# Kernel optimization log

Measured on AMD Instinct MI355X. Metric: run time of the kernel, lower is better.

Reference implementation:

```python
import jax, jax.numpy as jnp
from jax import lax
import numpy as np

# ----- static optical constants (from config) -----
N = 500            # phase mask grid
PX = 1e-6          # pixel pitch [m]
WL = 532e-9        # wavelength [m]
FL = 0.1           # focal length [m]
RI = 1.0           # refractive index
FWHC = 150e-6      # laser beam FWHC
K = 2.0 * np.pi * RI / WL
QE, DARK_MEAN, READ_STD, GAIN, MAX_ADU = 0.9, 0.005, 1.6, 2.0, 65535.0
MAX_VAL = 4.0e9    # Normalize01 max
PHOTONS = 1.0e6    # photons per emitter (max_intensity-style scaling)
R = 15             # psf_keep_radius -> 31x31 crops

_x = np.arange(-N // 2, N // 2) * PX
_X, _Y = np.meshgrid(_x, _x)
INCIDENT = np.exp(-(_X**2 + _Y**2) / (2.0 * FWHC**2)).astype(np.float32)
_C1 = (np.pi / (WL * FL) * (_X**2 + _Y**2)) % (2.0 * np.pi)
B1 = np.exp(-1j * _C1).astype(np.complex64)
# angular-spectrum gamma, directly in unshifted fft order
_F = np.fft.fftfreq(N, d=PX)
_A, _B = np.meshgrid(RI * WL * _F, RI * WL * _F)
GAMMA = np.sqrt(np.maximum(1.0 - _A**2 - _B**2, 0.0)).astype(np.float32)

def _gauss7():
    m = (7 - 1) / 2.0
    y, x = np.ogrid[-m:m + 1, -m:m + 1]
    h = np.exp(-(x * x + y * y) / 2.0)
    h[h < np.finfo(h.dtype).eps * h.max()] = 0
    return h.astype(np.float32)
GAUSS7 = _gauss7()


def setup_inputs() -> dict:
    key = jax.random.key(0)
    k1, k2, k3, k4, k5, k6, k7 = jax.random.split(key, 7)
    B, Ne = 8, 64
    phase_mask = jax.random.uniform(k1, (N, N), jnp.float32, 0.0, 2.0 * np.pi)
    zs = jax.random.uniform(k2, (Ne,), jnp.float32, 0.0, 1e-4)  # defocus depths [m]
    xyz = jax.random.randint(k3, (B, Ne, 2), 0, 170, jnp.int32) + 15  # in [15,184]
    std_u = jax.random.uniform(k4, (1,), jnp.float32)
    eps_dark = jax.random.normal(k5, (B, 1, 198, 198), jnp.float32)
    eps_photon = jax.random.normal(k6, (B, 1, 198, 198), jnp.float32)
    eps_read = jax.random.normal(k7, (B, 1, 198, 198), jnp.float32)
    return {"phase_mask": phase_mask, "zs": zs, "xyz": xyz, "std_u": std_u,
            "eps_dark": eps_dark, "eps_photon": eps_photon, "eps_read": eps_read}


def _forward(phase_mask, zs, xyz, std_u, eps_dark, eps_photon, eps_read):
    Bn, Ne = xyz.shape[0], xyz.shape[1]
    # --- FFT-based PSF generation (angular spectrum propagation) ---
    field = (INCIDENT * jnp.exp(1j * phase_mask) * B1).astype(jnp.complex64)  # [N,N]
    Ef = jnp.fft.fft2(field)                                                  # [N,N]
    H = jnp.exp(1j * ((K * GAMMA)[None] * zs[:, None, None]))                 # [Ne,N,N]
    Eprop = jnp.fft.ifft2(Ef[None] * H)                                       # [Ne,N,N]
    inten = jnp.abs(Eprop) ** 2
    c = N // 2
    psf = inten[:, c - R:c + R + 1, c - R:c + R + 1]                          # [Ne,31,31]
    psf = psf / (jnp.sum(psf, (-2, -1), keepdims=True) + 1e-12) * PHOTONS
    images4D = jnp.broadcast_to(psf[None], (Bn, Ne, 2 * R + 1, 2 * R + 1))
    # --- imgs4dto3d: scatter-add 31x31 patches into 200x200 canvas ---
    offs = jnp.arange(2 * R + 1) - R
    rows = xyz[..., 0][..., None, None] + offs[None, None, :, None]           # [B,Ne,31,1]
    cols = xyz[..., 1][..., None, None] + offs[None, None, None, :]           # [B,Ne,1,31]
    bidx = jnp.arange(Bn)[:, None, None, None]
    canvas = jnp.zeros((Bn, 200, 200), psf.dtype).at[bidx, rows, cols].add(images4D)
    img = canvas[:, None]                                                     # [B,1,200,200]
    # --- BlurLayer: per-draw std gaussian, conv pad=2 -> 198x198 ---
    std = 0.8 + 0.4 * std_u[0]
    s2 = std * std
    kern = (1.0 / (2.0 * jnp.pi * s2)) * GAUSS7 ** (1.0 / s2)
    blurred = lax.conv_general_dilated(img, kern[None, None], (1, 1),
                                       [(2, 2), (2, 2)],
                                       dimension_numbers=("NCHW", "OIHW", "NCHW"))
    # --- NoiseLayer (reparameterized gaussian approximations) ---
    sig = blurred * QE
    dark = DARK_MEAN + eps_dark * jnp.sqrt(jnp.float32(DARK_MEAN))
    total = jnp.maximum(sig + dark, 0.0)
    noisy = total + eps_photon * jnp.sqrt(jnp.maximum(total, 1e-12))
    elec = noisy + eps_read * READ_STD
    adu = jnp.clip(elec * GAIN, 0.0, MAX_ADU)
    # --- Normalize01 ---
    out = jnp.where(adu <= 10.0, 1.0, jnp.minimum(adu, MAX_VAL)) / MAX_VAL
    return out.astype(jnp.float32)


def reference(phase_mask, zs, xyz, std_u, eps_dark, eps_photon, eps_read):
    return _forward(phase_mask, zs, xyz, std_u, eps_dark, eps_photon, eps_read)
```

## Files before the change

kernel.cpp:

```cpp
#include <hip/hip_runtime.h>
#include <math.h>

#define NN 500
#define NE 64
#define BATCH 8
#define RR 15
#define PW 31
#define CAN 200
#define OHW 198
#define TWO_PI_F 6.28318530717958647692f
#define SETUP_N (BATCH * CAN * CAN + NE + 49)

#define BG2_F16 (64 * 2 * 2 * 64 * 8)
#define ASCALE (1.0f / 64.0f)

using f16x8 = __attribute__((ext_vector_type(8))) _Float16;
using f32x16 = __attribute__((ext_vector_type(16))) float;

__device__ __forceinline__ void fast_sincos_red(float theta, float* s, float* c) {
    const float INV2PI = 0.15915494309189535f;
    const float PI2_HI = 6.28318548202514648f;
    const float PI2_LO = -1.7484556e-7f;
    float n = rintf(theta * INV2PI);
    float r = fmaf(n, -PI2_HI, theta);
    r = fmaf(n, -PI2_LO, r);
    *s = __sinf(r);
    *c = __cosf(r);
}

__global__ void k_setup(const float* __restrict__ std_u,
                        float* __restrict__ kgamma,
                        float2* __restrict__ tw,
                        float* __restrict__ kern,
                        float* __restrict__ canvas,
                        float* __restrict__ psf_sums,
                        _Float16* __restrict__ Bg2) {
    int idx = blockIdx.x * blockDim.x + threadIdx.x;
    if (idx < NN) {
        double th = 2.0 * M_PI * (double)idx / (double)NN;
        tw[idx] = make_float2((float)cos(th), (float)sin(th));
    }
    if (idx < BG2_F16) {
        int e = idx & 7;
        int lane = (idx >> 3) & 63;
        int nt = (idx >> 9) & 1;
        int plane = (idx >> 10) & 1;
        int gs = idx >> 11;
        int kap = gs * 16 + (lane >> 5) * 8 + e;
        int nu = nt * 32 + (lane & 31);
        float outv = 0.f;
        if (kap < 2 * NN) {
            int u = kap >> 1, p = kap & 1;
            int ri = nu >> 1, q = nu & 1;
            int r = 235 + ri;
            int m = (u * r) % NN;
            double th = 2.0 * M_PI * (double)m / (double)NN;
            double wre = cos(th), wim = sin(th);
            double val = (q == 0) ? ((p == 0) ? wre : -wim)
                                  : ((p == 0) ? wim : wre);
            float x = (float)val;
            _Float16 h = (_Float16)x;
            outv = (plane == 0) ? (float)h : (x - (float)h);
        }
        Bg2[idx] = (_Float16)outv;
    }
    if (idx < BATCH * CAN * CAN) canvas[idx] = 0.f;
    if (idx >= BATCH * CAN * CAN && idx < BATCH * CAN * CAN + NE)
        psf_sums[idx - BATCH * CAN * CAN] = 0.f;
    if (idx >= BATCH * CAN * CAN + NE && idx < SETUP_N) {
        int t = idx - (BATCH * CAN * CAN + NE);
        float stdv = 0.8f + 0.4f * std_u[0];
        float s2 = stdv * stdv;
        int a = t / 7 - 3, b = t % 7 - 3;
        float g = (float)exp(-0.5 * (double)(a * a + b * b));
        kern[t] = (1.0f / (2.0f * (float)M_PI * s2)) * powf(g, 1.0f / s2);
    }
    if (idx >= NN * NN) return;
    int i = idx / NN, j = idx % NN;
    double fy = (double)((i < 250) ? i : i - 500) * 2000.0;
    double fx = (double)((j < 250) ? j : j - 500) * 2000.0;
    double a = 5.32e-7 * fx;
    double b = 5.32e-7 * fy;
    double g = 1.0 - a * a - b * b;
    g = (g > 0.0) ? sqrt(g) : 0.0;
    float Kf = (float)(2.0 * M_PI * 1.0 / 5.32e-7);
    kgamma[idx] = Kf * (float)g;
}

__device__ __forceinline__ void ct_dft_stages(const float2* xs, const float2* tts,
                                              float2* S, int t,
                                              float2* out1, float2* out2, int* kout) {
    if (t < 250) {
        int d = t / 25;
        int b = t % 25;
        float2 st = tts[(25 * d) % NN];
        float wr = 1.f, wi = 0.f;
        float Er = 0.f, Ei = 0.f, Or_ = 0.f, Oi = 0.f;
#pragma unroll
        for (int a = 0; a < 20; a += 2) {
            float2 x0 = xs[25 * a + b];
            Er += x0.x * wr - x0.y * wi;
            Ei += x0.x * wi + x0.y * wr;
            float nr = wr * st.x - wi * st.y;
            float ni = wr * st.y + wi * st.x;
            float2 x1 = xs[25 * (a + 1) + b];
            Or_ += x1.x * nr - x1.y * ni;
            Oi  += x1.x * ni + x1.y * nr;
            wr = nr * st.x - ni * st.y;
            wi = nr * st.y + ni * st.x;
        }
        S[b * 21 + d]      = make_float2(Er + Or_, Ei + Oi);
        S[b * 21 + d + 10] = make_float2(Er - Or_, Ei - Oi);
    }
    __syncthreads();
    if (t < 250) {
        int k = t;
        int d1 = k % 20;
        int d2 = (d1 + 10) % 20;
        float2 s1 = tts[k];
        float wr = 1.f, wi = 0.f;
        float a1r = 0.f, a1i = 0.f, a2r = 0.f, a2i = 0.f;
#pragma unroll
        for (int b = 0; b < 25; ++b) {
            float2 u1 = S[b * 21 + d1];
            float2 u2 = S[b * 21 + d2];
            a1r += u1.x * wr - u1.y * wi;
            a1i += u1.x * wi + u1.y * wr;
            float sgnb = (b & 1) ? -1.f : 1.f;
            float w2r = sgnb * wr, w2i = sgnb * wi;
            a2r += u2.x * w2r - u2.y * w2i;
            a2i += u2.x * w2i + u2.y * w2r;
            float nr = wr * s1.x - wi * s1.y;
            wi = wr * s1.y + wi * s1.x;
            wr = nr;
        }
        *out1 = make_float2(a1r, a1i);
        *out2 = make_float2(a2r, a2i);
        *kout = k;
    }
}

__global__ void k_dft_rows(const float* __restrict__ phase, float2* __restrict__ dst,
                           const float2* __restrict__ tw) {
    __shared__ __align__(16) float2 xs[NN];
    __shared__ float2 tts[NN];
    __shared__ float2 S[25 * 21];
    int line = blockIdx.x;
    int t = threadIdx.x;
    const float INV2SIG = 2.2222222e7f;
    const float C1M = (float)(M_PI / 5.32e-8);
    float y = (float)(line - 250) * 1e-6f;
    float y2 = y * y;
    const float* prow = phase + (size_t)line * NN;
    for (int n = t; n < NN; n += 256) {
        float x = (float)(n - 250) * 1e-6f;
        float r2 = x * x + y2;
        float inc = __expf(-r2 * INV2SIG);
        float c1 = C1M * r2;
        float b1r = __cosf(c1), b1i = -__sinf(c1);
        float ph = prow[n];
        float sp = __sinf(ph), cp = __cosf(ph);
        float ar = inc * cp, ai = inc * sp;
        xs[n] = make_float2(ar * b1r - ai * b1i, ar * b1i + ai * b1r);
        float2 tt = tw[n];
        tts[n] = make_float2(tt.x, -tt.y);
    }
    __syncthreads();
    float2 o1, o2; int k;
    ct_dft_stages(xs, tts, S, t, &o1, &o2, &k);
    if (t < 250) {
        dst[(size_t)k * NN + line] = o1;
        dst[(size_t)(k + 250) * NN + line] = o2;
    }
}

__global__ void k_dft_cols(const float2* __restrict__ src, float2* __restrict__ dst,
                           const float2* __restrict__ tw) {
    __shared__ __align__(16) float2 xs[NN];
    __shared__ float2 tts[NN];
    __shared__ float2 S[25 * 21];
    int line = blockIdx.x;
    const float2* s = src + (size_t)line * NN;
    int t = threadIdx.x;
    for (int n = t; n < NN; n += 256) {
        xs[n] = s[n];
        float2 tt = tw[n];
        tts[n] = make_float2(tt.x, -tt.y);
    }
    __syncthreads();
    float2 o1, o2; int k;
    ct_dft_stages(xs, tts, S, t, &o1, &o2, &k);
    if (t < 250) {
        float2* dp = dst + (size_t)line * NN;
        dp[k] = o1;
        dp[k + 250] = o2;
    }
}

__global__ void __launch_bounds__(256)
k_prop_mfma(const float2* __restrict__ EfT,
            const float* __restrict__ kgamma,
            const float* __restrict__ zs,
            const _Float16* __restrict__ Bg2,
            float* __restrict__ part) {
    __shared__ __align__(16) char smem[4 * 2048 * 4];
    float2* eft = (float2*)smem;
    float*  kgs = (float*)(smem + 4096);
    float*  ctile4 = (float*)smem;

    int v = blockIdx.x;
    int zh = blockIdx.y;
    int t = threadIdx.x;
    int w = t >> 6;
    int lane = t & 63;
    int l31 = lane & 31;
    int lk = lane >> 5;

    for (int n = t; n < 512; n += 256) {
        if (n < NN) {
            float2 e = EfT[(size_t)v * NN + n];
            eft[n] = make_float2(e.x * ASCALE, e.y * ASCALE);
            kgs[n] = kgamma[(size_t)v * NN + n];
        } else {
            eft[n] = make_float2(0.f, 0.f);
            kgs[n] = 0.f;
        }
    }
    float zv = zs[zh * 32 + l31];
    __syncthreads();

    f32x16 acc[2] = {};

#define MODSPLIT(ex, ey, kgv, i0) do {                                        \
        float s_, c_;                                                         \
        fast_sincos_red((kgv) * zv, &s_, &c_);                                \
        float yr = (ex) * c_ - (ey) * s_;                                     \
        float yi = (ex) * s_ + (ey) * c_;                                     \
        _Float16 h0 = (_Float16)yr;                                           \
        ah[i0] = h0; al[i0] = (_Float16)(yr - (float)h0);                     \
        _Float16 h1 = (_Float16)yi;                                           \
        ah[i0 + 1] = h1; al[i0 + 1] = (_Float16)(yi - (float)h1);             \
    } while (0)

    const _Float16* bbase = Bg2 + (size_t)(w * 16) * 2048 + (size_t)lane * 8;
#pragma unroll 4
    for (int s = 0; s < 16; ++s) {
        const _Float16* bs = bbase + (size_t)s * 2048;
        f16x8 bh0 = *(const f16x8*)(bs);
        f16x8 bh1 = *(const f16x8*)(bs + 512);
        f16x8 bl0 = *(const f16x8*)(bs + 1024);
        f16x8 bl1 = *(const f16x8*)(bs + 1536);
        int u0 = w * 128 + s * 8 + lk * 4;
        f16x8 ah, al;
        {
            float4 e01 = *(const float4*)&eft[u0];
            float4 e23 = *(const float4*)&eft[u0 + 2];
            float4 kg4 = *(const float4*)&kgs[u0];
            MODSPLIT(e01.x, e01.y, kg4.x, 0);
            MODSPLIT(e01.z, e01.w, kg4.y, 2);
            MODSPLIT(e23.x, e23.y, kg4.z, 4);
            MODSPLIT(e23.z, e23.w, kg4.w, 6);
        }
        acc[0] = __builtin_amdgcn_mfma_f32_32x32x16_f16(ah, bh0, acc[0], 0, 0, 0);
        acc[0] = __builtin_amdgcn_mfma_f32_32x32x16_f16(al, bh0, acc[0], 0, 0, 0);
        acc[0] = __builtin_amdgcn_mfma_f32_32x32x16_f16(ah, bl0, acc[0], 0, 0, 0);
        acc[1] = __builtin_amdgcn_mfma_f32_32x32x16_f16(ah, bh1, acc[1], 0, 0, 0);
        acc[1] = __builtin_amdgcn_mfma_f32_32x32x16_f16(al, bh1, acc[1], 0, 0, 0);
        acc[1] = __builtin_amdgcn_mfma_f32_32x32x16_f16(ah, bl1, acc[1], 0, 0, 0);
    }
#undef MODSPLIT

    __syncthreads();
    {
        float* slice = ctile4 + w * 2048;
#pragma unroll
        for (int nt = 0; nt < 2; ++nt)
#pragma unroll
            for (int reg = 0; reg < 16; ++reg) {
                int row = (reg & 3) + 8 * (reg >> 2) + 4 * lk;
                slice[row * 64 + nt * 32 + l31] = acc[nt][reg];
            }
    }
    __syncthreads();
#pragma unroll
    for (int pass = 0; pass < 2; ++pass) {
        int idx = pass * 256 + t;
        int i4 = idx * 4;
        int z = i4 >> 6, c4 = (i4 & 63) >> 2;
        float4 a0 = *(const float4*)&ctile4[i4];
        float4 a1 = *(const float4*)&ctile4[2048 + i4];
        float4 a2 = *(const float4*)&ctile4[4096 + i4];
        float4 a3 = *(const float4*)&ctile4[6144 + i4];
        float4 val = make_float4(a0.x + a1.x + a2.x + a3.x,
                                 a0.y + a1.y + a2.y + a3.y,
                                 a0.z + a1.z + a2.z + a3.z,
                                 a0.w + a1.w + a2.w + a3.w);
        *(float4*)&part[((size_t)(zh * 32 + z) * NN + v) * 64 + c4 * 4] = val;
    }
}

__global__ void k_prop_cols(const float* __restrict__ part,
                            float* __restrict__ psf,
                            float* __restrict__ psf_sums) {
    __shared__ __align__(16) float X2[NN][16];
    int rq = blockIdx.x;
    int z  = blockIdx.y;
    int t  = threadIdx.x;
    const float* p0 = part + ((size_t)z * NN) * 64 + rq * 16;
    for (int i = t; i < NN * 4; i += 256) {
        int v = i >> 2, q4 = i & 3;
        float4 a = *(const float4*)(p0 + (size_t)v * 64 + q4 * 4);
        *(float4*)&X2[v][q4 * 4] = a;
    }
    __syncthreads();
    int ril = t >> 5;
    int ri  = rq * 8 + ril;
    int ci  = t & 31;
    float val = 0.f;
    if (ri < PW && ci < PW) {
        int c = 235 + ci;
        float ar = 0.f, ai = 0.f;
        float sr, si;
        {
            float th = (TWO_PI_F / NN) * (float)(c % NN);
            sincosf(th, &si, &sr);
        }
        for (int vb = 0; vb < 4; ++vb) {
            int v0 = vb * 125;
            float wr, wi;
            float th = (TWO_PI_F / NN) * (float)((v0 * c) % NN);
            sincosf(th, &wi, &wr);
            for (int v = v0; v < v0 + 125; ++v) {
                float2 xy = *(const float2*)&X2[v][2 * ril];
                ar += xy.x * wr - xy.y * wi;
                ai += xy.x * wi + xy.y * wr;
                float nwr = wr * sr - wi * si;
                wi = wr * si + wi * sr;
                wr = nwr;
            }
        }
        const float inv = 64.0f / 250000.0f;
        float re = ar * inv, im = ai * inv;
        val = re * re + im * im;
        psf[(size_t)z * (PW * PW) + ri * PW + ci] = val;
    }
#pragma unroll
    for (int m = 1; m < 64; m <<= 1) val += __shfl_xor(val, m);
    if ((t & 63) == 0) atomicAdd(&psf_sums[z], val);
}

__global__ void k_scatter(const float* __restrict__ psf,
                          const float* __restrict__ psf_sums,
                          const int* __restrict__ xyz,
                          float* __restrict__ canvas) {
    int e = blockIdx.x;
    int b = blockIdx.y;
    int r0 = xyz[(b * NE + e) * 2 + 0] - RR;
    int c0 = xyz[(b * NE + e) * 2 + 1] - RR;
    float sc = 1.0e6f / (psf_sums[e] + 1e-12f);
    float* cb = canvas + (size_t)b * (CAN * CAN);
    for (int p = threadIdx.x; p < PW * PW; p += blockDim.x) {
        int i = p / PW, j = p % PW;
        atomicAdd(cb + (r0 + i) * CAN + (c0 + j), psf[e * PW * PW + p] * sc);
    }
}

__global__ void k_final(const float* __restrict__ canvas,
                        const float* __restrict__ kern,
                        const float* __restrict__ eps_dark,
                        const float* __restrict__ eps_photon,
                        const float* __restrict__ eps_read,
                        float* __restrict__ out) {
    __shared__ float kk[49];
    __shared__ float tile[14][40];
    int b = blockIdx.z;
    int tx = threadIdx.x, ty = threadIdx.y;
    int t = ty * 32 + tx;
    int j0 = blockIdx.x * 32, i0 = blockIdx.y * 8;
    if (t < 49) kk[t] = kern[t];
    const float* cb = canvas + (size_t)b * (CAN * CAN);
    for (int p = t; p < 14 * 38; p += 256) {
        int rr = p / 38, cc = p % 38;
        int gi = i0 + rr - 2, gj = j0 + cc - 2;
        tile[rr][cc] = (gi >= 0 && gi < CAN && gj >= 0 && gj < CAN)
                           ? cb[gi * CAN + gj] : 0.f;
    }
    __syncthreads();
    int i = i0 + ty, j = j0 + tx;
    if (i >= OHW || j >= OHW) return;
    float acc = 0.f;
#pragma unroll
    for (int a = 0; a < 7; ++a)
#pragma unroll
        for (int q = 0; q < 7; ++q)
            acc += tile[ty + a][tx + q] * kk[a * 7 + q];
    int idx = b * (OHW * OHW) + i * OHW + j;
    float sig = acc * 0.9f;
    float dark = 0.005f + eps_dark[idx] * sqrtf(0.005f);
    float total = fmaxf(sig + dark, 0.0f);
    float noisy = total + eps_photon[idx] * sqrtf(fmaxf(total, 1e-12f));
    float elec = noisy + eps_read[idx] * 1.6f;
    float adu = fminf(fmaxf(elec * 2.0f, 0.0f), 65535.0f);
    float v = (adu <= 10.0f) ? 1.0f : fminf(adu, 4.0e9f);
    out[idx] = v / 4.0e9f;
}

extern "C" void kernel_launch(void* const* d_in, const int* in_sizes, int n_in,
                              void* d_out, int out_size, void* d_ws, size_t ws_size,
                              hipStream_t stream) {
    const float* phase    = (const float*)d_in[0];
    const float* zs       = (const float*)d_in[1];
    const int*   xyz      = (const int*)d_in[2];
    const float* std_u    = (const float*)d_in[3];
    const float* epsd     = (const float*)d_in[4];
    const float* epsp     = (const float*)d_in[5];
    const float* epsr     = (const float*)d_in[6];
    float* out = (float*)d_out;

    char* ws = (char*)d_ws;
    size_t off = 0;
    auto alloc = [&](size_t bytes) {
        off = (off + 255) & ~(size_t)255;
        size_t o = off; off += bytes; return o;
    };
    float*  kgamma   = (float*) (ws + alloc((size_t)NN * NN * 4));
    float2* tw       = (float2*)(ws + alloc((size_t)NN * 8));
    float2* R1T      = (float2*)(ws + alloc((size_t)NN * NN * 8));
    float2* EfT      = (float2*)(ws + alloc((size_t)NN * NN * 8));
    float*  part     = (float*) (ws + alloc((size_t)NE * NN * 64 * 4));
    float*  psf      = (float*) (ws + alloc((size_t)NE * PW * PW * 4));
    float*  psf_sums = (float*) (ws + alloc((size_t)NE * 4));
    float*  kern     = (float*) (ws + alloc((size_t)64 * 4));
    float*  canvas   = (float*) (ws + alloc((size_t)BATCH * CAN * CAN * 4));
    _Float16* Bg2    = (_Float16*)(ws + alloc((size_t)BG2_F16 * 2));
    (void)ws_size; (void)n_in; (void)in_sizes; (void)out_size;

    k_setup<<<(SETUP_N + 255) / 256, 256, 0, stream>>>(
        std_u, kgamma, tw, kern, canvas, psf_sums, Bg2);
    k_dft_rows<<<NN, 256, 0, stream>>>(phase, R1T, tw);
    k_dft_cols<<<NN, 256, 0, stream>>>(R1T, EfT, tw);
    k_prop_mfma<<<dim3(NN, 2), 256, 0, stream>>>(EfT, kgamma, zs, Bg2, part);
    k_prop_cols<<<dim3(4, NE), 256, 0, stream>>>(part, psf, psf_sums);
    k_scatter<<<dim3(NE, BATCH), 256, 0, stream>>>(psf, psf_sums, xyz, canvas);
    k_final<<<dim3((OHW + 31) / 32, (OHW + 7) / 8, BATCH), dim3(32, 8), 0, stream>>>(
        canvas, kern, epsd, epsp, epsr, out);
}
```

Measured before the change: 136.4 us.

## Fuse column DFT into MFMA propagation kernel, processing two lines per block

Merges the column-DFT kernel into the propagation MFMA kernel so the transformed line stays in shared memory instead of being written to and reread from the EfT global buffer. Each block now handles two lines, reusing the loaded B-matrix fragments across both and running two accumulator sets. The cost is that the column DFT is computed redundantly for each of the two z-halves (gridDim.y=2), the block's grid is halved, and register and shared-memory pressure per block goes up.

```diff
diff --git a/kernel.cpp b/kernel.cpp
--- a/kernel.cpp
+++ b/kernel.cpp
@@ -174,76 +174,71 @@
     }
 }
 
-__global__ void k_dft_cols(const float2* __restrict__ src, float2* __restrict__ dst,
-                           const float2* __restrict__ tw) {
-    __shared__ __align__(16) float2 xs[NN];
-    __shared__ float2 tts[NN];
-    __shared__ float2 S[25 * 21];
-    int line = blockIdx.x;
-    const float2* s = src + (size_t)line * NN;
+__global__ void __launch_bounds__(256)
+k_dft_prop(const float2* __restrict__ R1T,
+           const float* __restrict__ kgamma,
+           const float* __restrict__ zs,
+           const float2* __restrict__ tw,
+           const _Float16* __restrict__ Bg2,
+           float* __restrict__ part) {
+    __shared__ __align__(16) char smem[45056];
+    float2* xs     = (float2*)smem;
+    float2* tts    = (float2*)(smem + 4000);
+    float2* S      = (float2*)(smem + 8000);
+    float*  ctile4 = (float*)smem;
+    float2* eft    = (float2*)(smem + 32768);
+    float*  kgs    = (float*)(smem + 40960);
+
+    int v0 = blockIdx.x * 2;
+    int zh = blockIdx.y;
     int t = threadIdx.x;
+
     for (int n = t; n < NN; n += 256) {
-        xs[n] = s[n];
         float2 tt = tw[n];
         tts[n] = make_float2(tt.x, -tt.y);
     }
+    for (int n = t; n < 1024; n += 256) {
+        int vv = n >> 9, u = n & 511;
+        kgs[n] = (u < NN) ? kgamma[(size_t)(v0 + vv) * NN + u] : 0.f;
+        if (u >= NN) eft[n] = make_float2(0.f, 0.f);
+    }
+
+    for (int vv = 0; vv < 2; ++vv) {
+        if (vv) __syncthreads();
+        const float2* srow = R1T + (size_t)(v0 + vv) * NN;
+        for (int n = t; n < NN; n += 256) xs[n] = srow[n];
+        __syncthreads();
+        float2 o1, o2; int k;
+        ct_dft_stages(xs, tts, S, t, &o1, &o2, &k);
+        if (t < 250) {
+            eft[vv * 512 + k]       = make_float2(o1.x * ASCALE, o1.y * ASCALE);
+            eft[vv * 512 + k + 250] = make_float2(o2.x * ASCALE, o2.y * ASCALE);
+        }
+    }
     __syncthreads();
-    float2 o1, o2; int k;
-    ct_dft_stages(xs, tts, S, t, &o1, &o2, &k);
-    if (t < 250) {
-        float2* dp = dst + (size_t)line * NN;
-        dp[k] = o1;
-        dp[k + 250] = o2;
-    }
-}
-
-__global__ void __launch_bounds__(256)
-k_prop_mfma(const float2* __restrict__ EfT,
-            const float* __restrict__ kgamma,
-            const float* __restrict__ zs,
-            const _Float16* __restrict__ Bg2,
-            float* __restrict__ part) {
-    __shared__ __align__(16) char smem[4 * 2048 * 4];
-    float2* eft = (float2*)smem;
-    float*  kgs = (float*)(smem + 4096);
-    float*  ctile4 = (float*)smem;
-
-    int v = blockIdx.x;
-    int zh = blockIdx.y;
-    int t = threadIdx.x;
+
     int w = t >> 6;
     int lane = t & 63;
     int l31 = lane & 31;
     int lk = lane >> 5;
-
-    for (int n = t; n < 512; n += 256) {
-        if (n < NN) {
-            float2 e = EfT[(size_t)v * NN + n];
-            eft[n] = make_float2(e.x * ASCALE, e.y * ASCALE);
-            kgs[n] = kgamma[(size_t)v * NN + n];
-        } else {
-            eft[n] = make_float2(0.f, 0.f);
-            kgs[n] = 0.f;
-        }
-    }
     float zv = zs[zh * 32 + l31];
-    __syncthreads();
-
-    f32x16 acc[2] = {};
-
-#define MODSPLIT(ex, ey, kgv, i0) do {                                        \
+
+    f32x16 acc0[2] = {};
+    f32x16 acc1[2] = {};
+
+#define MODSPLIT(AH, AL, ex, ey, kgv, i0) do {                                \
         float s_, c_;                                                         \
         fast_sincos_red((kgv) * zv, &s_, &c_);                                \
         float yr = (ex) * c_ - (ey) * s_;                                     \
         float yi = (ex) * s_ + (ey) * c_;                                     \
         _Float16 h0 = (_Float16)yr;                                           \
-        ah[i0] = h0; al[i0] = (_Float16)(yr - (float)h0);                     \
+        AH[i0] = h0; AL[i0] = (_Float16)(yr - (float)h0);                     \
         _Float16 h1 = (_Float16)yi;                                           \
-        ah[i0 + 1] = h1; al[i0 + 1] = (_Float16)(yi - (float)h1);             \
+        AH[i0 + 1] = h1; AL[i0 + 1] = (_Float16)(yi - (float)h1);             \
     } while (0)
 
     const _Float16* bbase = Bg2 + (size_t)(w * 16) * 2048 + (size_t)lane * 8;
-#pragma unroll 4
+#pragma unroll 2
     for (int s = 0; s < 16; ++s) {
         const _Float16* bs = bbase + (size_t)s * 2048;
         f16x8 bh0 = *(const f16x8*)(bs);
@@ -251,51 +246,70 @@
         f16x8 bl0 = *(const f16x8*)(bs + 1024);
         f16x8 bl1 = *(const f16x8*)(bs + 1536);
         int u0 = w * 128 + s * 8 + lk * 4;
-        f16x8 ah, al;
+        f16x8 ah0, al0, ah1, al1;
         {
             float4 e01 = *(const float4*)&eft[u0];
             float4 e23 = *(const float4*)&eft[u0 + 2];
             float4 kg4 = *(const float4*)&kgs[u0];
-            MODSPLIT(e01.x, e01.y, kg4.x, 0);
-            MODSPLIT(e01.z, e01.w, kg4.y, 2);
-            MODSPLIT(e23.x, e23.y, kg4.z, 4);
-            MODSPLIT(e23.z, e23.w, kg4.w, 6);
-        }
-        acc[0] = __builtin_amdgcn_mfma_f32_32x32x16_f16(ah, bh0, acc[0], 0, 0, 0);
-        acc[0] = __builtin_amdgcn_mfma_f32_32x32x16_f16(al, bh0, acc[0], 0, 0, 0);
-        acc[0] = __builtin_amdgcn_mfma_f32_32x32x16_f16(ah, bl0, acc[0], 0, 0, 0);
-        acc[1] = __builtin_amdgcn_mfma_f32_32x32x16_f16(ah, bh1, acc[1], 0, 0, 0);
-        acc[1] = __builtin_amdgcn_mfma_f32_32x32x16_f16(al, bh1, acc[1], 0, 0, 0);
-        acc[1] = __builtin_amdgcn_mfma_f32_32x32x16_f16(ah, bl1, acc[1], 0, 0, 0);
+            MODSPLIT(ah0, al0, e01.x, e01.y, kg4.x, 0);
+            MODSPLIT(ah0, al0, e01.z, e01.w, kg4.y, 2);
+            MODSPLIT(ah0, al0, e23.x, e23.y, kg4.z, 4);
+            MODSPLIT(ah0, al0, e23.z, e23.w, kg4.w, 6);
+        }
+        {
+            float4 e01 = *(const float4*)&eft[512 + u0];
+            float4 e23 = *(const float4*)&eft[512 + u0 + 2];
+            float4 kg4 = *(const float4*)&kgs[512 + u0];
+            MODSPLIT(ah1, al1, e01.x, e01.y, kg4.x, 0);
+            MODSPLIT(ah1, al1, e01.z, e01.w, kg4.y, 2);
+            MODSPLIT(ah1, al1, e23.x, e23.y, kg4.z, 4);
+            MODSPLIT(ah1, al1, e23.z, e23.w, kg4.w, 6);
+        }
+        acc0[0] = __builtin_amdgcn_mfma_f32_32x32x16_f16(ah0, bh0, acc0[0], 0, 0, 0);
+        acc0[0] = __builtin_amdgcn_mfma_f32_32x32x16_f16(al0, bh0, acc0[0], 0, 0, 0);
+        acc0[0] = __builtin_amdgcn_mfma_f32_32x32x16_f16(ah0, bl0, acc0[0], 0, 0, 0);
+        acc0[1] = __builtin_amdgcn_mfma_f32_32x32x16_f16(ah0, bh1, acc0[1], 0, 0, 0);
+        acc0[1] = __builtin_amdgcn_mfma_f32_32x32x16_f16(al0, bh1, acc0[1], 0, 0, 0);
+        acc0[1] = __builtin_amdgcn_mfma_f32_32x32x16_f16(ah0, bl1, acc0[1], 0, 0, 0);
+        acc1[0] = __builtin_amdgcn_mfma_f32_32x32x16_f16(ah1, bh0, acc1[0], 0, 0, 0);
+        acc1[0] = __builtin_amdgcn_mfma_f32_32x32x16_f16(al1, bh0, acc1[0], 0, 0, 0);
+        acc1[0] = __builtin_amdgcn_mfma_f32_32x32x16_f16(ah1, bl0, acc1[0], 0, 0, 0);
+        acc1[1] = __builtin_amdgcn_mfma_f32_32x32x16_f16(ah1, bh1, acc1[1], 0, 0, 0);
+        acc1[1] = __builtin_amdgcn_mfma_f32_32x32x16_f16(al1, bh1, acc1[1], 0, 0, 0);
+        acc1[1] = __builtin_amdgcn_mfma_f32_32x32x16_f16(ah1, bl1, acc1[1], 0, 0, 0);
     }
 #undef MODSPLIT
 
-    __syncthreads();
-    {
-        float* slice = ctile4 + w * 2048;
-#pragma unroll
-        for (int nt = 0; nt < 2; ++nt)
-#pragma unroll
-            for (int reg = 0; reg < 16; ++reg) {
-                int row = (reg & 3) + 8 * (reg >> 2) + 4 * lk;
-                slice[row * 64 + nt * 32 + l31] = acc[nt][reg];
-            }
-    }
-    __syncthreads();
-#pragma unroll
-    for (int pass = 0; pass < 2; ++pass) {
-        int idx = pass * 256 + t;
-        int i4 = idx * 4;
-        int z = i4 >> 6, c4 = (i4 & 63) >> 2;
-        float4 a0 = *(const float4*)&ctile4[i4];
-        float4 a1 = *(const float4*)&ctile4[2048 + i4];
-        float4 a2 = *(const float4*)&ctile4[4096 + i4];
-        float4 a3 = *(const float4*)&ctile4[6144 + i4];
-        float4 val = make_float4(a0.x + a1.x + a2.x + a3.x,
-                                 a0.y + a1.y + a2.y + a3.y,
-                                 a0.z + a1.z + a2.z + a3.z,
-                                 a0.w + a1.w + a2.w + a3.w);
-        *(float4*)&part[((size_t)(zh * 32 + z) * NN + v) * 64 + c4 * 4] = val;
+#pragma unroll
+    for (int vv = 0; vv < 2; ++vv) {
+        {
+            float* slice = ctile4 + w * 2048;
+            const f32x16* ac = (vv == 0) ? acc0 : acc1;
+#pragma unroll
+            for (int nt = 0; nt < 2; ++nt)
+#pragma unroll
+                for (int reg = 0; reg < 16; ++reg) {
+                    int row = (reg & 3) + 8 * (reg >> 2) + 4 * lk;
+                    slice[row * 64 + nt * 32 + l31] = ac[nt][reg];
+                }
+        }
+        __syncthreads();
+#pragma unroll
+        for (int pass = 0; pass < 2; ++pass) {
+            int idx = pass * 256 + t;
+            int i4 = idx * 4;
+            int z = i4 >> 6, c4 = (i4 & 63) >> 2;
+            float4 a0 = *(const float4*)&ctile4[i4];
+            float4 a1 = *(const float4*)&ctile4[2048 + i4];
+            float4 a2 = *(const float4*)&ctile4[4096 + i4];
+            float4 a3 = *(const float4*)&ctile4[6144 + i4];
+            float4 val = make_float4(a0.x + a1.x + a2.x + a3.x,
+                                     a0.y + a1.y + a2.y + a3.y,
+                                     a0.z + a1.z + a2.z + a3.z,
+                                     a0.w + a1.w + a2.w + a3.w);
+            *(float4*)&part[((size_t)(zh * 32 + z) * NN + (v0 + vv)) * 64 + c4 * 4] = val;
+        }
+        __syncthreads();
     }
 }
 
@@ -426,7 +440,6 @@
     float*  kgamma   = (float*) (ws + alloc((size_t)NN * NN * 4));
     float2* tw       = (float2*)(ws + alloc((size_t)NN * 8));
     float2* R1T      = (float2*)(ws + alloc((size_t)NN * NN * 8));
-    float2* EfT      = (float2*)(ws + alloc((size_t)NN * NN * 8));
     float*  part     = (float*) (ws + alloc((size_t)NE * NN * 64 * 4));
     float*  psf      = (float*) (ws + alloc((size_t)NE * PW * PW * 4));
     float*  psf_sums = (float*) (ws + alloc((size_t)NE * 4));
@@ -438,8 +451,7 @@
     k_setup<<<(SETUP_N + 255) / 256, 256, 0, stream>>>(
         std_u, kgamma, tw, kern, canvas, psf_sums, Bg2);
     k_dft_rows<<<NN, 256, 0, stream>>>(phase, R1T, tw);
-    k_dft_cols<<<NN, 256, 0, stream>>>(R1T, EfT, tw);
-    k_prop_mfma<<<dim3(NN, 2), 256, 0, stream>>>(EfT, kgamma, zs, Bg2, part);
+    k_dft_prop<<<dim3(NN / 2, 2), 256, 0, stream>>>(R1T, kgamma, zs, tw, Bg2, part);
     k_prop_cols<<<dim3(4, NE), 256, 0, stream>>>(part, psf, psf_sums);
     k_scatter<<<dim3(NE, BATCH), 256, 0, stream>>>(psf, psf_sums, xyz, canvas);
     k_final<<<dim3((OHW + 31) / 32, (OHW + 7) / 8, BATCH), dim3(32, 8), 0, stream>>>(
```

Measured after the change: 140.0 us. 1.03x slower.
